# Optimization experiments

Hardware: AMD Instinct MI355X
Metric: run time of the kernel (lower is better)

Reference implementation:

```python
import jax, jax.numpy as jnp
import numpy as np

N, F_IN, F_OUT = 8192, 256, 256
ALPHA = 0.2  # LeakyReLU negative slope
NEG = -9e15

def setup_inputs() -> dict:
    key = jax.random.key(0)
    k1, k2, k3, k4, k5 = jax.random.split(key, 5)
    h = jax.random.normal(k1, (N, F_IN), dtype=jnp.float32)
    adj = jax.random.randint(k2, (N, N), 0, 2, dtype=jnp.int32)
    W_w = jax.random.normal(k3, (F_IN, F_OUT), dtype=jnp.float32) / np.sqrt(F_IN)
    W_b = jax.random.normal(k4, (F_OUT,), dtype=jnp.float32) * 0.01
    a = jax.random.normal(k5, (2 * F_OUT, 1), dtype=jnp.float32) / np.sqrt(2 * F_OUT)
    return {"h": h, "adj": adj, "W_w": W_w, "W_b": W_b, "a": a}

def reference(h, adj, W_w, W_b, a):
    # Wh: [N, F_OUT]
    Wh = h @ W_w + W_b
    a1 = a[:F_OUT, 0]   # scores for source node i (row)
    a2 = a[F_OUT:, 0]   # scores for target node j (col)
    # e[i,j] = leakyrelu(Wh_i . a1 + Wh_j . a2)  -- separable form of the
    # original repeat/cat construction, identical math without the NxNx2F tensor.
    e = jax.nn.leaky_relu((Wh @ a1)[:, None] + (Wh @ a2)[None, :], negative_slope=ALPHA)
    attention = jnp.where(adj > 0, e, NEG)
    attention = jax.nn.softmax(attention, axis=1)
    # dropout is identity in eval / p=0
    h_prime = attention @ Wh  # [N, F_OUT]
    return h_prime
```

## Files before the change

kernel.cpp:

```cpp
#include <hip/hip_runtime.h>
#include <stdint.h>

#define NN 8192
#define FD 256
#define LOG2E 1.44269504088896340736f
#define SPLIT 4
#define JSLICE (NN / SPLIT)
#define JCH 32
#define NCH (JSLICE / JCH)
#define PST 40

typedef __attribute__((ext_vector_type(8))) __bf16 bf16x8;
typedef __attribute__((ext_vector_type(4))) float f32x4;

__device__ __forceinline__ unsigned short f2bf(float x) {
    unsigned u = __float_as_uint(x);
    u = u + 0x7fffu + ((u >> 16) & 1u);
    return (unsigned short)(u >> 16);
}
__device__ __forceinline__ bf16x8 ld_bf8(const unsigned short* p) {
    uint4 v = *(const uint4*)p;
    return __builtin_bit_cast(bf16x8, v);
}
__device__ __forceinline__ void async_ld16(const int* g, int* lds_base) {
    __builtin_amdgcn_global_load_lds(
        (const __attribute__((address_space(1))) void*)g,
        (__attribute__((address_space(3))) void*)lds_base, 16, 0, 0);
}

__global__ __launch_bounds__(256) void wtrans_kernel(const float* __restrict__ W,
                                                     unsigned short* __restrict__ WbT) {
    int idx = blockIdx.x * 256 + threadIdx.x;
    int k = idx >> 8, f = idx & 255;
    WbT[f * 256 + k] = f2bf(W[idx]);
}

__global__ __launch_bounds__(256) void gemm1_kernel(const float* __restrict__ h,
                                                    const unsigned short* __restrict__ WbT,
                                                    const float* __restrict__ bias,
                                                    const float* __restrict__ av,
                                                    unsigned short* __restrict__ WhT,
                                                    float* __restrict__ f1p,
                                                    float* __restrict__ f2p) {
    __shared__ float Wh_s[256 * 33];
    __shared__ float red_s[2 * 8 * 32];
    int t = threadIdx.x;
    int l = t & 63, w = t >> 6;
    int i0 = blockIdx.x * 32;
    int fbase = w * 64;
    int cl = l & 15, q = l >> 4;

    f32x4 acc[2][4] = {};
    const float* hA0 = h + (size_t)(i0 + cl) * FD;
    const float* hA1 = h + (size_t)(i0 + 16 + cl) * FD;

    #pragma unroll
    for (int ks = 0; ks < 8; ++ks) {
        int kk = ks * 32 + q * 8;
        union { unsigned short u[8]; bf16x8 v; } ua0, ua1;
        float4 x0 = *(const float4*)(hA0 + kk);
        float4 x1 = *(const float4*)(hA0 + kk + 4);
        float4 y0 = *(const float4*)(hA1 + kk);
        float4 y1 = *(const float4*)(hA1 + kk + 4);
        ua0.u[0]=f2bf(x0.x); ua0.u[1]=f2bf(x0.y); ua0.u[2]=f2bf(x0.z); ua0.u[3]=f2bf(x0.w);
        ua0.u[4]=f2bf(x1.x); ua0.u[5]=f2bf(x1.y); ua0.u[6]=f2bf(x1.z); ua0.u[7]=f2bf(x1.w);
        ua1.u[0]=f2bf(y0.x); ua1.u[1]=f2bf(y0.y); ua1.u[2]=f2bf(y0.z); ua1.u[3]=f2bf(y0.w);
        ua1.u[4]=f2bf(y1.x); ua1.u[5]=f2bf(y1.y); ua1.u[6]=f2bf(y1.z); ua1.u[7]=f2bf(y1.w);
        #pragma unroll
        for (int bg = 0; bg < 4; ++bg) {
            bf16x8 bF = ld_bf8(WbT + (fbase + bg * 16 + cl) * 256 + kk);
            acc[0][bg] = __builtin_amdgcn_mfma_f32_16x16x32_bf16(ua0.v, bF, acc[0][bg], 0, 0, 0);
            acc[1][bg] = __builtin_amdgcn_mfma_f32_16x16x32_bf16(ua1.v, bF, acc[1][bg], 0, 0, 0);
        }
    }

    #pragma unroll
    for (int mt = 0; mt < 2; ++mt)
        #pragma unroll
        for (int bg = 0; bg < 4; ++bg)
            #pragma unroll
            for (int e = 0; e < 4; ++e) {
                int il = mt * 16 + q * 4 + e;
                int fl = fbase + bg * 16 + cl;
                Wh_s[fl * 33 + il] = acc[mt][bg][e] + bias[fl];
            }
    __syncthreads();
    {
        const float* src = &Wh_s[t * 33];
        unsigned short* dst = WhT + (size_t)t * NN + i0;
        #pragma unroll
        for (int ig = 0; ig < 4; ++ig) {
            union { unsigned short u[8]; uint4 v; } p;
            #pragma unroll
            for (int e = 0; e < 8; ++e) p.u[e] = f2bf(src[ig * 8 + e]);
            *(uint4*)(dst + ig * 8) = p.v;
        }
    }
    {
        int i = t & 31, fc = t >> 5;
        float s1 = 0.f, s2 = 0.f;
        #pragma unroll
        for (int fo = 0; fo < 32; ++fo) {
            int f = fc * 32 + fo;
            float wv = Wh_s[f * 33 + i];
            s1 += wv * av[f];
            s2 += wv * av[256 + f];
        }
        red_s[fc * 32 + i] = s1;
        red_s[256 + fc * 32 + i] = s2;
    }
    __syncthreads();
    if (t < 32) {
        float s = 0.f;
        #pragma unroll
        for (int fc = 0; fc < 8; ++fc) s += red_s[fc * 32 + t];
        f1p[i0 + t] = s * LOG2E;
    } else if (t < 64) {
        int i = t - 32;
        float s = 0.f;
        #pragma unroll
        for (int fc = 0; fc < 8; ++fc) s += red_s[256 + fc * 32 + i];
        f2p[i0 + i] = s * LOG2E;
    }
}

__global__ __launch_bounds__(256, 4) void gat_kernel(const int* __restrict__ adj,
                                                     const unsigned short* __restrict__ WhT,
                                                     const float* __restrict__ f1p,
                                                     const float* __restrict__ f2p,
                                                     float* __restrict__ num,
                                                     float* __restrict__ den) {
    __shared__ __align__(16) int adj_s[2][1024];
    __shared__ __align__(16) unsigned short P_s[2][32 * PST];

    int t = threadIdx.x;
    int l = t & 63, w = t >> 6;
    int strip = blockIdx.x & 255;
    int s = blockIdx.x >> 8;
    int i0 = strip * 32;
    int j0 = s * JSLICE;

    int prow = w * 8 + (l >> 3);
    int pcol = (l & 7) * 4;
    float f1v = f1p[i0 + prow];
    const int* agl = adj + (size_t)(i0 + prow) * NN + j0 + pcol;

    int cl = l & 15, q = l >> 4;
    int fbase = w * 64;
    const unsigned short* wrowb = WhT + (size_t)(fbase + cl) * NN + j0 + q * 8;

    f32x4 acc[2][4] = {};
    float rs = 0.f;
    float4 f2n;
    bf16x8 bcur[4], bnext[4];

    async_ld16(agl, &adj_s[0][w * 256]);
    f2n = *(const float4*)(f2p + j0 + pcol);

    #pragma unroll 2
    for (int jt = 0; jt <= NCH; ++jt) {
        int b = jt & 1;
        __syncthreads();
        if (jt + 1 < NCH) async_ld16(agl + (jt + 1) * JCH, &adj_s[b ^ 1][w * 256]);

        if (jt < NCH) {
            int4 a4 = *(const int4*)&adj_s[b][t * 4];
            float4 fv = f2n;
            if (jt + 1 < NCH) f2n = *(const float4*)(f2p + j0 + (jt + 1) * JCH + pcol);
            float fa[4] = {fv.x, fv.y, fv.z, fv.w};
            int ad[4] = {a4.x, a4.y, a4.z, a4.w};
            unsigned short pu[4];
            #pragma unroll
            for (int e = 0; e < 4; ++e) {
                float sv = f1v + fa[e];
                sv = fmaxf(sv, 0.2f * sv);
                float wv = exp2f(sv);
                wv = ad[e] > 0 ? wv : 0.f;
                rs += wv;
                pu[e] = f2bf(wv);
            }
            *(uint2*)&P_s[b][prow * PST + pcol] =
                make_uint2((unsigned)pu[0] | ((unsigned)pu[1] << 16),
                           (unsigned)pu[2] | ((unsigned)pu[3] << 16));
            #pragma unroll
            for (int bg = 0; bg < 4; ++bg)
                bnext[bg] = ld_bf8(wrowb + (size_t)bg * 16 * NN + jt * JCH);
        }
        if (jt > 0) {
            const unsigned short* ps = P_s[b ^ 1];
            bf16x8 af0 = ld_bf8(ps + cl * PST + q * 8);
            bf16x8 af1 = ld_bf8(ps + (16 + cl) * PST + q * 8);
            #pragma unroll
            for (int bg = 0; bg < 4; ++bg) {
                acc[0][bg] = __builtin_amdgcn_mfma_f32_16x16x32_bf16(af0, bcur[bg], acc[0][bg], 0, 0, 0);
                acc[1][bg] = __builtin_amdgcn_mfma_f32_16x16x32_bf16(af1, bcur[bg], acc[1][bg], 0, 0, 0);
            }
        }
        #pragma unroll
        for (int bg = 0; bg < 4; ++bg) bcur[bg] = bnext[bg];
    }

    rs += __shfl_xor(rs, 1);
    rs += __shfl_xor(rs, 2);
    rs += __shfl_xor(rs, 4);
    if ((l & 7) == 0) den[(size_t)s * NN + i0 + prow] = rs;

    float* nrow = num + (size_t)s * NN * FD;
    #pragma unroll
    for (int mt = 0; mt < 2; ++mt)
        #pragma unroll
        for (int e = 0; e < 4; ++e) {
            int r = mt * 16 + q * 4 + e;
            #pragma unroll
            for (int bg = 0; bg < 4; ++bg)
                nrow[(size_t)(i0 + r) * FD + fbase + bg * 16 + cl] = acc[mt][bg][e];
        }
}

__global__ __launch_bounds__(256) void combine_kernel(const float* __restrict__ num,
                                                      const float* __restrict__ den,
                                                      float* __restrict__ out) {
    int idx = blockIdx.x * 256 + threadIdx.x;
    int i = idx >> 8;
    float nsum = 0.f, dsum = 0.f;
    #pragma unroll
    for (int s = 0; s < SPLIT; ++s) {
        nsum += num[(size_t)s * NN * FD + idx];
        dsum += den[(size_t)s * NN + i];
    }
    out[idx] = nsum / dsum;
}

extern "C" void kernel_launch(void* const* d_in, const int* in_sizes, int n_in,
                              void* d_out, int out_size, void* d_ws, size_t ws_size,
                              hipStream_t stream) {
    const float* h   = (const float*)d_in[0];
    const int*   adj = (const int*)d_in[1];
    const float* W   = (const float*)d_in[2];
    const float* b   = (const float*)d_in[3];
    const float* a   = (const float*)d_in[4];
    float* out = (float*)d_out;

    char* ws = (char*)d_ws;
    unsigned short* WhT = (unsigned short*)ws;
    unsigned short* WbT = (unsigned short*)(ws + (4u << 20));
    float* f1p = (float*)(ws + (4u << 20) + (128u << 10));
    float* f2p = f1p + NN;
    float* den = f2p + NN;
    float* num = (float*)(ws + (8u << 20));

    wtrans_kernel<<<256, 256, 0, stream>>>(W, WbT);
    gemm1_kernel<<<256, 256, 0, stream>>>(h, WbT, b, a, WhT, f1p, f2p);
    gat_kernel<<<256 * SPLIT, 256, 0, stream>>>(adj, WhT, f1p, f2p, num, den);
    combine_kernel<<<NN * FD / 256, 256, 0, stream>>>(num, den, out);
}
```

Baseline: 503.7 us.

## Compute attention weights directly in MFMA A-fragment registers, drop LDS staging

The GAT kernel is restructured so each lane computes the softmax weights for exactly the A-operand elements it feeds to the bf16 MFMA. The weights are packed straight into registers with a truncating perm-based bf16 conversion, which removes the LDS adjacency buffer, the P staging buffer, the async global-to-LDS loads and the per-iteration __syncthreads. Work is split as 2 row groups by 2 feature halves with 8 accumulators per wave, so each wave now recomputes exp for its rows and reloads adjacency redundantly across the feature halves. It also loses the explicit software prefetch of the B operand and changes rounding from round-to-nearest to truncation.

```diff
diff --git a/kernel.cpp b/kernel.cpp
--- a/kernel.cpp
+++ b/kernel.cpp
@@ -6,9 +6,7 @@
 #define LOG2E 1.44269504088896340736f
 #define SPLIT 4
 #define JSLICE (NN / SPLIT)
-#define JCH 32
-#define NCH (JSLICE / JCH)
-#define PST 40
+#define NIT (JSLICE / 32)
 
 typedef __attribute__((ext_vector_type(8))) __bf16 bf16x8;
 typedef __attribute__((ext_vector_type(4))) float f32x4;
@@ -22,10 +20,8 @@
     uint4 v = *(const uint4*)p;
     return __builtin_bit_cast(bf16x8, v);
 }
-__device__ __forceinline__ void async_ld16(const int* g, int* lds_base) {
-    __builtin_amdgcn_global_load_lds(
-        (const __attribute__((address_space(1))) void*)g,
-        (__attribute__((address_space(3))) void*)lds_base, 16, 0, 0);
+__device__ __forceinline__ unsigned pack_trunc2(float a, float b) {
+    return __builtin_amdgcn_perm(__float_as_uint(b), __float_as_uint(a), 0x07060302u);
 }
 
 __global__ __launch_bounds__(256) void wtrans_kernel(const float* __restrict__ W,
@@ -130,9 +126,6 @@
                                                      const float* __restrict__ f2p,
                                                      float* __restrict__ num,
                                                      float* __restrict__ den) {
-    __shared__ __align__(16) int adj_s[2][1024];
-    __shared__ __align__(16) unsigned short P_s[2][32 * PST];
-
     int t = threadIdx.x;
     int l = t & 63, w = t >> 6;
     int strip = blockIdx.x & 255;
@@ -140,81 +133,64 @@
     int i0 = strip * 32;
     int j0 = s * JSLICE;
 
-    int prow = w * 8 + (l >> 3);
-    int pcol = (l & 7) * 4;
-    float f1v = f1p[i0 + prow];
-    const int* agl = adj + (size_t)(i0 + prow) * NN + j0 + pcol;
-
     int cl = l & 15, q = l >> 4;
-    int fbase = w * 64;
-    const unsigned short* wrowb = WhT + (size_t)(fbase + cl) * NN + j0 + q * 8;
-
-    f32x4 acc[2][4] = {};
+    int roff = (w >> 1) * 16;
+    int fbase = (w & 1) * 128;
+
+    float f1v = f1p[i0 + roff + cl];
+    const int* arow = adj + (size_t)(i0 + roff + cl) * NN + j0 + q * 8;
+    const float* f2row = f2p + j0 + q * 8;
+    const unsigned short* wb = WhT + (size_t)(fbase + cl) * NN + j0 + q * 8;
+
+    f32x4 acc[8] = {};
     float rs = 0.f;
-    float4 f2n;
-    bf16x8 bcur[4], bnext[4];
-
-    async_ld16(agl, &adj_s[0][w * 256]);
-    f2n = *(const float4*)(f2p + j0 + pcol);
 
     #pragma unroll 2
-    for (int jt = 0; jt <= NCH; ++jt) {
-        int b = jt & 1;
-        __syncthreads();
-        if (jt + 1 < NCH) async_ld16(agl + (jt + 1) * JCH, &adj_s[b ^ 1][w * 256]);
-
-        if (jt < NCH) {
-            int4 a4 = *(const int4*)&adj_s[b][t * 4];
-            float4 fv = f2n;
-            if (jt + 1 < NCH) f2n = *(const float4*)(f2p + j0 + (jt + 1) * JCH + pcol);
-            float fa[4] = {fv.x, fv.y, fv.z, fv.w};
-            int ad[4] = {a4.x, a4.y, a4.z, a4.w};
-            unsigned short pu[4];
-            #pragma unroll
-            for (int e = 0; e < 4; ++e) {
-                float sv = f1v + fa[e];
-                sv = fmaxf(sv, 0.2f * sv);
-                float wv = exp2f(sv);
-                wv = ad[e] > 0 ? wv : 0.f;
-                rs += wv;
-                pu[e] = f2bf(wv);
-            }
-            *(uint2*)&P_s[b][prow * PST + pcol] =
-                make_uint2((unsigned)pu[0] | ((unsigned)pu[1] << 16),
-                           (unsigned)pu[2] | ((unsigned)pu[3] << 16));
-            #pragma unroll
-            for (int bg = 0; bg < 4; ++bg)
-                bnext[bg] = ld_bf8(wrowb + (size_t)bg * 16 * NN + jt * JCH);
-        }
-        if (jt > 0) {
-            const unsigned short* ps = P_s[b ^ 1];
-            bf16x8 af0 = ld_bf8(ps + cl * PST + q * 8);
-            bf16x8 af1 = ld_bf8(ps + (16 + cl) * PST + q * 8);
-            #pragma unroll
-            for (int bg = 0; bg < 4; ++bg) {
-                acc[0][bg] = __builtin_amdgcn_mfma_f32_16x16x32_bf16(af0, bcur[bg], acc[0][bg], 0, 0, 0);
-                acc[1][bg] = __builtin_amdgcn_mfma_f32_16x16x32_bf16(af1, bcur[bg], acc[1][bg], 0, 0, 0);
-            }
-        }
-        #pragma unroll
-        for (int bg = 0; bg < 4; ++bg) bcur[bg] = bnext[bg];
-    }
-
-    rs += __shfl_xor(rs, 1);
-    rs += __shfl_xor(rs, 2);
-    rs += __shfl_xor(rs, 4);
-    if ((l & 7) == 0) den[(size_t)s * NN + i0 + prow] = rs;
+    for (int jt = 0; jt < NIT; ++jt) {
+        int jo = jt * 32;
+        int4 a0 = *(const int4*)(arow + jo);
+        int4 a1 = *(const int4*)(arow + jo + 4);
+        float4 F0 = *(const float4*)(f2row + jo);
+        float4 F1 = *(const float4*)(f2row + jo + 4);
+
+        float fe[8] = {F0.x, F0.y, F0.z, F0.w, F1.x, F1.y, F1.z, F1.w};
+        int   ae[8] = {a0.x, a0.y, a0.z, a0.w, a1.x, a1.y, a1.z, a1.w};
+        float wv[8];
+        #pragma unroll
+        for (int e = 0; e < 8; ++e) {
+            float sv = f1v + fe[e];
+            sv = fmaxf(sv, 0.2f * sv);
+            float x = __builtin_amdgcn_exp2f(sv);
+            x = ae[e] > 0 ? x : 0.f;
+            rs += x;
+            wv[e] = x;
+        }
+        union { unsigned u[4]; bf16x8 v; } af;
+        af.u[0] = pack_trunc2(wv[0], wv[1]);
+        af.u[1] = pack_trunc2(wv[2], wv[3]);
+        af.u[2] = pack_trunc2(wv[4], wv[5]);
+        af.u[3] = pack_trunc2(wv[6], wv[7]);
+
+        #pragma unroll
+        for (int bg = 0; bg < 8; ++bg) {
+            bf16x8 bF = ld_bf8(wb + (size_t)(bg * 16) * NN + jo);
+            acc[bg] = __builtin_amdgcn_mfma_f32_16x16x32_bf16(af.v, bF, acc[bg], 0, 0, 0);
+        }
+    }
+
+    rs += __shfl_xor(rs, 16);
+    rs += __shfl_xor(rs, 32);
+    if ((w & 1) == 0 && l < 16)
+        den[(size_t)s * NN + i0 + roff + l] = rs;
 
     float* nrow = num + (size_t)s * NN * FD;
     #pragma unroll
-    for (int mt = 0; mt < 2; ++mt)
-        #pragma unroll
-        for (int e = 0; e < 4; ++e) {
-            int r = mt * 16 + q * 4 + e;
-            #pragma unroll
-            for (int bg = 0; bg < 4; ++bg)
-                nrow[(size_t)(i0 + r) * FD + fbase + bg * 16 + cl] = acc[mt][bg][e];
-        }
+    for (int e = 0; e < 4; ++e) {
+        int r = roff + q * 4 + e;
+        #pragma unroll
+        for (int bg = 0; bg < 8; ++bg)
+            nrow[(size_t)(i0 + r) * FD + fbase + bg * 16 + cl] = acc[bg][e];
+    }
 }
 
 __global__ __launch_bounds__(256) void combine_kernel(const float* __restrict__ num,
```

Measured after the change: 618.1 us. +22.7%, slower.
